# Optimization experiments

Hardware: AMD Instinct MI355X
Metric: run time of the kernel (lower is better)

Reference implementation:

```python
import jax, jax.numpy as jnp
import numpy as np
from jax.scipy.special import gammaln

ORDER = 16          # spline order -> ORDER+1 basis columns
SUPP0, SUPP1 = 0.0, 1.0  # support interval
N_POINTS = 4_000_000


def setup_inputs() -> dict:
    key = jax.random.key(0)
    # evaluation points, one scalar per row, inside the support
    x = jax.random.uniform(key, (N_POINTS, 1), dtype=jnp.float32)
    return {"x": x}


def _beta_pdf_nz(y, a, b):
    # Beta(a,b).prob(y) = y^(a-1) (1-y)^(b-1) / B(a,b), with nan/inf -> 0
    # (matches tf_nan_to_zero applied to tfp Beta.prob; a=0 or b=0 gives
    #  lbeta=+inf -> logpdf=-inf -> pdf=0, nans at edges are zeroed)
    lbeta = gammaln(a) + gammaln(b) - gammaln(a + b)
    logpdf = (a - 1.0) * jnp.log(y) + (b - 1.0) * jnp.log1p(-y) - lbeta
    p = jnp.exp(logpdf)
    return jnp.where(jnp.isfinite(p), p, 0.0)


def reference(x):
    x = x.astype(jnp.float32)
    scale = SUPP1 - SUPP0
    y = (x - SUPP0) / scale                      # [N, 1], in [0,1]
    m = jnp.arange(ORDER + 1, dtype=jnp.float32)  # [ORDER+1]
    # vectorized over all m at once (original loops over m and concats)
    first = _beta_pdf_nz(y, m, ORDER - m + 1.0)  # [N, ORDER+1]
    sec = _beta_pdf_nz(y, m + 1.0, ORDER - m)    # [N, ORDER+1]
    return (first - sec) / scale                 # [N, ORDER+1]
```

## Files before the change

kernel.cpp:

```cpp
#include <hip/hip_runtime.h>

#define NCOL 17
#define BLK  256
#define TILE_FLOATS (BLK * NCOL)
#define TILE_VEC4   (TILE_FLOATS / 4)
#define MAX_GRID    2048

__global__ __launch_bounds__(BLK) void bsp_prime_kernel(
    const float* __restrict__ x, float* __restrict__ out, int n) {
    const float C15[16] = {1.f, 15.f, 105.f, 455.f, 1365.f, 3003.f, 5005.f, 6435.f,
                           6435.f, 5005.f, 3003.f, 1365.f, 455.f, 105.f, 15.f, 1.f};

    __shared__ float tile[TILE_FLOATS];

    const int t = threadIdx.x;
    const int ntiles = (n + BLK - 1) / BLK;
    const long long total = (long long)n * NCOL;

    for (int tb = blockIdx.x; tb < ntiles; tb += gridDim.x) {
        const int i = tb * BLK + t;
        float y = (i < n) ? x[i] : 0.5f;
        const bool edge = (y <= 0.0f) || (y >= 1.0f);
        const float omy = 1.0f - y;

        float yp[NCOL], op[NCOL];
        yp[0] = 1.0f;
        op[0] = 1.0f;
#pragma unroll
        for (int k = 1; k < NCOL; ++k) {
            yp[k] = yp[k - 1] * y;
            op[k] = op[k - 1] * omy;
        }

        float f[NCOL + 1];
        f[0] = 0.0f;
        f[NCOL] = 0.0f;
#pragma unroll
        for (int m = 1; m <= 16; ++m) {
            f[m] = C15[m - 1] * yp[m - 1] * op[16 - m];
        }

        __syncthreads();
#pragma unroll
        for (int m = 0; m < NCOL; ++m) {
            float v = 16.0f * (f[m] - f[m + 1]);
            tile[t * NCOL + m] = edge ? 0.0f : v;
        }
        __syncthreads();

        const long long base = (long long)tb * TILE_FLOATS;
        if (base + TILE_FLOATS <= total) {
            const float4* __restrict__ s4 = (const float4*)tile;
            float4* __restrict__ o4 = (float4*)(out + base);
#pragma unroll
            for (int k = 0; k < 4; ++k) {
                o4[k * BLK + t] = s4[k * BLK + t];
            }
            if (t < TILE_VEC4 - 4 * BLK) {
                o4[4 * BLK + t] = s4[4 * BLK + t];
            }
        } else {
            for (int k = 0; k < NCOL; ++k) {
                long long idx = base + (long long)k * BLK + t;
                if (idx < total) out[idx] = tile[k * BLK + t];
            }
        }
    }
}

extern "C" void kernel_launch(void* const* d_in, const int* in_sizes, int n_in,
                              void* d_out, int out_size, void* d_ws, size_t ws_size,
                              hipStream_t stream) {
    const float* x = (const float*)d_in[0];
    float* out = (float*)d_out;
    const int n = in_sizes[0];
    const int ntiles = (n + BLK - 1) / BLK;
    const int grid = ntiles < MAX_GRID ? ntiles : MAX_GRID;
    bsp_prime_kernel<<<grid, BLK, 0, stream>>>(x, out, n);
}
```

Baseline: 280.9 us.

## Use per-wavefront LDS tiles and drop block-wide barriers

Each 64-lane wavefront now owns a private shared-memory tile and walks its own stream of 64-point chunks. Because a wavefront runs its lanes together, the block-wide __syncthreads around the LDS transpose are removed, which lets waves progress independently instead of stalling each other. The factor 16 is folded into the binomial coefficient table, saving one multiply per column. The correctness relies on wave-synchronous LDS ordering within a wavefront and on the compiler not reordering the LDS stores and loads.

Measured after the change: 281.3 us. About the same (+0.1%).

```diff
diff --git a/kernel.cpp b/kernel.cpp
--- a/kernel.cpp
+++ b/kernel.cpp
@@ -1,24 +1,34 @@
 #include <hip/hip_runtime.h>
 
 #define NCOL 17
+#define WAVE 64
 #define BLK  256
-#define TILE_FLOATS (BLK * NCOL)
-#define TILE_VEC4   (TILE_FLOATS / 4)
-#define MAX_GRID    2048
+#define WPB  (BLK / WAVE)
+#define WTILE (WAVE * NCOL)
+#define WVEC4 (WTILE / 4)
+#define MAX_GRID 2048
 
 __global__ __launch_bounds__(BLK) void bsp_prime_kernel(
     const float* __restrict__ x, float* __restrict__ out, int n) {
-    const float C15[16] = {1.f, 15.f, 105.f, 455.f, 1365.f, 3003.f, 5005.f, 6435.f,
-                           6435.f, 5005.f, 3003.f, 1365.f, 455.f, 105.f, 15.f, 1.f};
+    const float C15x16[16] = {16.f,    240.f,   1680.f,  7280.f,
+                              21840.f, 48048.f, 80080.f, 102960.f,
+                              102960.f, 80080.f, 48048.f, 21840.f,
+                              7280.f,  1680.f,  240.f,   16.f};
 
-    __shared__ float tile[TILE_FLOATS];
+    __shared__ float tile[WPB][WTILE];
 
     const int t = threadIdx.x;
-    const int ntiles = (n + BLK - 1) / BLK;
+    const int w = t >> 6;
+    const int l = t & 63;
+    float* __restrict__ wt = tile[w];
+
+    const int ntiles = (n + WAVE - 1) / WAVE;
     const long long total = (long long)n * NCOL;
+    const int wid0 = blockIdx.x * WPB + w;
+    const int wstride = gridDim.x * WPB;
 
-    for (int tb = blockIdx.x; tb < ntiles; tb += gridDim.x) {
-        const int i = tb * BLK + t;
+    for (int tb = wid0; tb < ntiles; tb += wstride) {
+        const int i = tb * WAVE + l;
         float y = (i < n) ? x[i] : 0.5f;
         const bool edge = (y <= 0.0f) || (y >= 1.0f);
         const float omy = 1.0f - y;
@@ -37,32 +47,29 @@
         f[NCOL] = 0.0f;
 #pragma unroll
         for (int m = 1; m <= 16; ++m) {
-            f[m] = C15[m - 1] * yp[m - 1] * op[16 - m];
+            f[m] = C15x16[m - 1] * yp[m - 1] * op[16 - m];
         }
 
-        __syncthreads();
 #pragma unroll
         for (int m = 0; m < NCOL; ++m) {
-            float v = 16.0f * (f[m] - f[m + 1]);
-            tile[t * NCOL + m] = edge ? 0.0f : v;
+            wt[l * NCOL + m] = edge ? 0.0f : (f[m] - f[m + 1]);
         }
-        __syncthreads();
 
-        const long long base = (long long)tb * TILE_FLOATS;
-        if (base + TILE_FLOATS <= total) {
-            const float4* __restrict__ s4 = (const float4*)tile;
+        const long long base = (long long)tb * WTILE;
+        if (base + WTILE <= total) {
+            const float4* __restrict__ s4 = (const float4*)wt;
             float4* __restrict__ o4 = (float4*)(out + base);
 #pragma unroll
             for (int k = 0; k < 4; ++k) {
-                o4[k * BLK + t] = s4[k * BLK + t];
+                o4[k * WAVE + l] = s4[k * WAVE + l];
             }
-            if (t < TILE_VEC4 - 4 * BLK) {
-                o4[4 * BLK + t] = s4[4 * BLK + t];
+            if (l < WVEC4 - 4 * WAVE) {
+                o4[4 * WAVE + l] = s4[4 * WAVE + l];
             }
         } else {
             for (int k = 0; k < NCOL; ++k) {
-                long long idx = base + (long long)k * BLK + t;
-                if (idx < total) out[idx] = tile[k * BLK + t];
+                long long idx = base + (long long)k * WAVE + l;
+                if (idx < total) out[idx] = wt[k * WAVE + l];
             }
         }
     }
@@ -74,7 +81,7 @@
     const float* x = (const float*)d_in[0];
     float* out = (float*)d_out;
     const int n = in_sizes[0];
-    const int ntiles = (n + BLK - 1) / BLK;
-    const int grid = ntiles < MAX_GRID ? ntiles : MAX_GRID;
+    const int nblocks = (n + BLK - 1) / BLK;
+    const int grid = nblocks < MAX_GRID ? nblocks : MAX_GRID;
     bsp_prime_kernel<<<grid, BLK, 0, stream>>>(x, out, n);
 }
```
